# Kernel tuning notes

Measured on AMD Instinct MI355X. Metric: run time of the kernel, lower is better.

Reference implementation:

```python
import jax, jax.numpy as jnp
import numpy as np
from jax import lax

DN = ('NCHW', 'OIHW', 'NCHW')

def binarize(w):
    # torch: w.sign().add(0.5).sign() maps w<0 -> -1, w>=0 -> +1 (0 -> +1)
    return jnp.where(w < 0, -1.0, 1.0).astype(w.dtype)

def bconv(x, w, b, dil):
    wb = binarize(w)
    y = lax.conv_general_dilated(x, wb, window_strides=(1, 1), padding='SAME',
                                 rhs_dilation=dil, dimension_numbers=DN)
    return y + b[None, :, None, None]

def setup_inputs() -> dict:
    key = jax.random.key(0)
    ks = jax.random.split(key, 9)
    C = 256
    Co = C // 4
    x = jax.random.normal(ks[0], (16, C, 128, 128), dtype=jnp.float32)
    w1 = jax.random.normal(ks[1], (Co, C, 1, 5), dtype=jnp.float32) * 0.05
    w2 = jax.random.normal(ks[2], (Co, C, 1, 5), dtype=jnp.float32) * 0.05
    w3 = jax.random.normal(ks[3], (Co, C, 5, 1), dtype=jnp.float32) * 0.05
    w4 = jax.random.normal(ks[4], (Co, C, 5, 1), dtype=jnp.float32) * 0.05
    b1 = jax.random.normal(ks[5], (Co,), dtype=jnp.float32) * 0.01
    b2 = jax.random.normal(ks[6], (Co,), dtype=jnp.float32) * 0.01
    b3 = jax.random.normal(ks[7], (Co,), dtype=jnp.float32) * 0.01
    b4 = jax.random.normal(ks[8], (Co,), dtype=jnp.float32) * 0.01
    return {'x': x, 'w1': w1, 'b1': b1, 'w2': w2, 'b2': b2,
            'w3': w3, 'b3': b3, 'w4': w4, 'b4': b4}

def reference(x, w1, b1, w2, b2, w3, b3, w4, b4):
    out1 = bconv(x, w1, b1, (1, 1))  # (1,5) dil 1
    out2 = bconv(x, w2, b2, (2, 2))  # (1,5) dil 2 (only W dim matters, H kernel=1)
    out3 = bconv(x, w3, b3, (1, 1))  # (5,1) dil 1
    out4 = bconv(x, w4, b4, (2, 2))  # (5,1) dil 2
    return jnp.concatenate([out1, out2, out3, out4], axis=1)
```

## Files before the change

### kernel.cpp

```cpp
#include <hip/hip_runtime.h>

typedef _Float16 half8  __attribute__((ext_vector_type(8)));
typedef float    floatx4 __attribute__((ext_vector_type(4)));

#define HW      128
#define CIN     256
#define NCHUNK  8
#define HALO_W  24
#define HALO_H  16
#define PITCH   20

__global__ void prep_weights(const float* __restrict__ w1,
                             const float* __restrict__ w2,
                             const float* __restrict__ w3,
                             const float* __restrict__ w4,
                             _Float16* __restrict__ wp)
{
    int idx  = blockIdx.x * 256 + threadIdx.x;
    int ci   = idx & 255;
    int rest = idx >> 8;
    int co   = rest & 63;
    int bt   = rest >> 6;
    int t    = bt % 5;
    int b    = bt / 5;
    const float* w = (b == 0) ? w1 : (b == 1) ? w2 : (b == 2) ? w3 : w4;
    float v = w[(co * 256 + ci) * 5 + t];
    wp[idx] = (v < 0.0f) ? (_Float16)(-1.0f) : (_Float16)(1.0f);
}

__global__ __launch_bounds__(256, 2)
void bconv_mfma(const float* __restrict__ x,
                const _Float16* __restrict__ wp,
                const float* __restrict__ bb1,
                const float* __restrict__ bb2,
                const float* __restrict__ bb3,
                const float* __restrict__ bb4,
                float* __restrict__ out)
{
    __shared__ __align__(16) unsigned int xs[HALO_H * HALO_W * PITCH];
    __shared__ float bias_s[256];

    const int tid  = threadIdx.x;
    const int w0t  = blockIdx.x * 16;
    const int h0t  = blockIdx.y * 8;
    const int nimg = blockIdx.z;

    {
        int br = tid >> 6, i = tid & 63;
        const float* bp = (br == 0) ? bb1 : (br == 1) ? bb2 : (br == 2) ? bb3 : bb4;
        bias_s[tid] = bp[i];
    }

    const int lane = tid & 63;
    const int wave = tid >> 6;
    const int quad = lane >> 4;
    const int wl   = lane & 15;

    floatx4 acc[4][8];
    #pragma unroll
    for (int m = 0; m < 4; ++m)
        #pragma unroll
        for (int n = 0; n < 8; ++n)
            acc[m][n] = (floatx4){0.f, 0.f, 0.f, 0.f};

    const int  dil   = (wave & 1) + 1;
    const bool horiz = (wave < 2);

    for (int chunk = 0; chunk < NCHUNK; ++chunk) {
        __syncthreads();

        #pragma unroll
        for (int s = 0; s < 6; ++s) {
            int u   = s * 256 + tid;
            int f   = u % 6;
            int g   = u / 6;
            int hh  = g & 15;
            int cp  = g >> 4;
            int ci0 = chunk * 32 + cp * 2;
            int hg  = h0t - 4 + hh;
            int wg  = w0t - 4 + f * 4;
            floatx4 v0 = {0.f,0.f,0.f,0.f}, v1 = {0.f,0.f,0.f,0.f};
            if (hg >= 0 && hg < HW && wg >= 0 && wg <= HW - 4) {
                const floatx4* p = (const floatx4*)(x + ((nimg * CIN + ci0) * HW + hg) * HW + wg);
                v0 = p[0];
                v1 = p[(HW * HW) / 4];
            }
            int pixb = hh * HALO_W + f * 4;
            #pragma unroll
            for (int i = 0; i < 4; ++i) {
                xs[(pixb + i) * PITCH + cp] =
                    __builtin_bit_cast(unsigned int,
                        __builtin_amdgcn_cvt_pkrtz(v0[i], v1[i]));
            }
        }
        __syncthreads();

        #pragma unroll
        for (int t = 0; t < 5; ++t) {
            half8 B[8];
            #pragma unroll
            for (int n = 0; n < 8; ++n) {
                int hh, ww;
                if (horiz) { hh = n + 4;                  ww = wl + 4 + (t - 2) * dil; }
                else       { hh = n + 4 + (t - 2) * dil;  ww = wl + 4; }
                B[n] = *(const half8*)&xs[(hh * HALO_W + ww) * PITCH + quad * 4];
            }
            #pragma unroll
            for (int m = 0; m < 4; ++m) {
                half8 A = *(const half8*)(wp +
                    (((wave * 5 + t) * 64 + m * 16 + wl) * 256 + chunk * 32 + quad * 8));
                #pragma unroll
                for (int n = 0; n < 8; ++n)
                    acc[m][n] = __builtin_amdgcn_mfma_f32_16x16x32_f16(A, B[n], acc[m][n], 0, 0, 0);
            }
        }
    }

    float bv[4][4];
    #pragma unroll
    for (int m = 0; m < 4; ++m)
        #pragma unroll
        for (int r = 0; r < 4; ++r)
            bv[m][r] = bias_s[wave * 64 + m * 16 + quad * 4 + r];

    #pragma unroll
    for (int m = 0; m < 4; ++m) {
        #pragma unroll
        for (int n = 0; n < 8; ++n) {
            int co   = wave * 64 + m * 16 + quad * 4;
            int base = ((nimg * 256 + co) * HW + (h0t + n)) * HW + w0t + wl;
            #pragma unroll
            for (int r = 0; r < 4; ++r)
                out[base + r * HW * HW] = acc[m][n][r] + bv[m][r];
        }
    }
}

extern "C" void kernel_launch(void* const* d_in, const int* in_sizes, int n_in,
                              void* d_out, int out_size, void* d_ws, size_t ws_size,
                              hipStream_t stream)
{
    (void)in_sizes; (void)n_in; (void)out_size; (void)ws_size;
    const float* x  = (const float*)d_in[0];
    const float* w1 = (const float*)d_in[1];
    const float* b1 = (const float*)d_in[2];
    const float* w2 = (const float*)d_in[3];
    const float* b2 = (const float*)d_in[4];
    const float* w3 = (const float*)d_in[5];
    const float* b3 = (const float*)d_in[6];
    const float* w4 = (const float*)d_in[7];
    const float* b4 = (const float*)d_in[8];
    float*    out = (float*)d_out;
    _Float16* wp  = (_Float16*)d_ws;

    prep_weights<<<1280, 256, 0, stream>>>(w1, w2, w3, w4, wp);

    dim3 grid(128 / 16, 128 / 8, 16);
    bconv_mfma<<<grid, dim3(256), 0, stream>>>(x, wp, b1, b2, b3, b4, out);
}
```

Baseline: 668.3 us.

## Split blocks by conv orientation, prefetch next chunk into registers, swizzle LDS

Each block now handles either the horizontal or the vertical branches, so the halo it loads is only one-sided (24x8 or 16x16 pixels) instead of the full 24x16 square. This removes the redundant loads of the old layout. The next channel chunk's global loads go into registers before the MFMA loop, overlapping memory latency with compute. Adding an XOR swizzle to the LDS layout is meant to reduce bank conflicts. Each wave's accumulators shrink to 4x4, which with launch bounds raised to 3 targets higher occupancy; in exchange the grid doubles and the A-weight loads are repeated across more blocks.

Result: slower. 1.050 ms (+57.1%).

```diff
diff --git a/kernel.cpp b/kernel.cpp
--- a/kernel.cpp
+++ b/kernel.cpp
@@ -3,12 +3,11 @@
 typedef _Float16 half8  __attribute__((ext_vector_type(8)));
 typedef float    floatx4 __attribute__((ext_vector_type(4)));
 
-#define HW      128
-#define CIN     256
-#define NCHUNK  8
-#define HALO_W  24
-#define HALO_H  16
-#define PITCH   20
+#define HW 128
+
+__device__ __forceinline__ int lds_word(int px, int cp) {
+    return px * 20 + (cp ^ (4 * ((px >> 3) & 3)));
+}
 
 __global__ void prep_weights(const float* __restrict__ w1,
                              const float* __restrict__ w2,
@@ -28,7 +27,7 @@
     wp[idx] = (v < 0.0f) ? (_Float16)(-1.0f) : (_Float16)(1.0f);
 }
 
-__global__ __launch_bounds__(256, 2)
+__global__ __launch_bounds__(256, 3)
 void bconv_mfma(const float* __restrict__ x,
                 const _Float16* __restrict__ wp,
                 const float* __restrict__ bb1,
@@ -37,12 +36,13 @@
                 const float* __restrict__ bb4,
                 float* __restrict__ out)
 {
-    __shared__ __align__(16) unsigned int xs[HALO_H * HALO_W * PITCH];
+    __shared__ __align__(16) unsigned int xs[5120];
     __shared__ float bias_s[256];
 
     const int tid  = threadIdx.x;
-    const int w0t  = blockIdx.x * 16;
-    const int h0t  = blockIdx.y * 8;
+    const int type = blockIdx.x & 1;
+    const int w0   = (blockIdx.x >> 1) * 16;
+    const int h0   = blockIdx.y * 8;
     const int nimg = blockIdx.z;
 
     {
@@ -51,66 +51,95 @@
         bias_s[tid] = bp[i];
     }
 
-    const int lane = tid & 63;
-    const int wave = tid >> 6;
-    const int quad = lane >> 4;
-    const int wl   = lane & 15;
+    const int lane   = tid & 63;
+    const int wave   = tid >> 6;
+    const int bi     = wave >> 1;
+    const int half   = wave & 1;
+    const int branch = type * 2 + bi;
+    const int dil    = bi + 1;
+    const int quad   = lane >> 4;
+    const int wl     = lane & 15;
 
-    floatx4 acc[4][8];
+    floatx4 acc[4][4];
     #pragma unroll
     for (int m = 0; m < 4; ++m)
         #pragma unroll
-        for (int n = 0; n < 8; ++n)
+        for (int n = 0; n < 4; ++n)
             acc[m][n] = (floatx4){0.f, 0.f, 0.f, 0.f};
 
-    const int  dil   = (wave & 1) + 1;
-    const bool horiz = (wave < 2);
+    const int NT = type ? 4 : 3;
+    int s_px[4], s_cp[4];
+    const float* s_ptr[4];
+    bool s_ok[4];
+    for (int s = 0; s < 4; ++s) {
+        int u = s * 256 + tid;
+        int f, hh, cp, wg, hg, rowpx;
+        if (type == 0) { f = u % 6;  hh = (u / 6) & 7;   cp = u / 48; wg = w0 - 4 + f * 4; hg = h0 + hh;     rowpx = 24; }
+        else           { f = u & 3;  hh = (u >> 2) & 15; cp = u >> 6; wg = w0 + f * 4;     hg = h0 - 4 + hh; rowpx = 16; }
+        if (cp > 15) cp = 15;
+        s_px[s]  = hh * rowpx + f * 4;
+        s_cp[s]  = cp;
+        s_ok[s]  = (wg >= 0) && (wg <= HW - 4) && (hg >= 0) && (hg < HW);
+        s_ptr[s] = x + (((long)(nimg * 256 + cp * 2) * HW + hg) * HW + wg);
+    }
 
-    for (int chunk = 0; chunk < NCHUNK; ++chunk) {
+    floatx4 R[8];
+
+    {
+        const int coff = 0;
+        for (int s = 0; s < NT; ++s) {
+            floatx4 a = {0.f,0.f,0.f,0.f}, b = {0.f,0.f,0.f,0.f};
+            if (s_ok[s]) {
+                const floatx4* p = (const floatx4*)(s_ptr[s] + coff);
+                a = p[0];
+                b = p[(HW * HW) / 4];
+            }
+            R[2 * s] = a; R[2 * s + 1] = b;
+        }
+    }
+
+    for (int c = 0; c < 8; ++c) {
         __syncthreads();
-
-        #pragma unroll
-        for (int s = 0; s < 6; ++s) {
-            int u   = s * 256 + tid;
-            int f   = u % 6;
-            int g   = u / 6;
-            int hh  = g & 15;
-            int cp  = g >> 4;
-            int ci0 = chunk * 32 + cp * 2;
-            int hg  = h0t - 4 + hh;
-            int wg  = w0t - 4 + f * 4;
-            floatx4 v0 = {0.f,0.f,0.f,0.f}, v1 = {0.f,0.f,0.f,0.f};
-            if (hg >= 0 && hg < HW && wg >= 0 && wg <= HW - 4) {
-                const floatx4* p = (const floatx4*)(x + ((nimg * CIN + ci0) * HW + hg) * HW + wg);
-                v0 = p[0];
-                v1 = p[(HW * HW) / 4];
-            }
-            int pixb = hh * HALO_W + f * 4;
+        for (int s = 0; s < NT; ++s) {
+            int base = s_px[s], cp = s_cp[s];
             #pragma unroll
-            for (int i = 0; i < 4; ++i) {
-                xs[(pixb + i) * PITCH + cp] =
+            for (int i = 0; i < 4; ++i)
+                xs[lds_word(base + i, cp)] =
                     __builtin_bit_cast(unsigned int,
-                        __builtin_amdgcn_cvt_pkrtz(v0[i], v1[i]));
-            }
+                        __builtin_amdgcn_cvt_pkrtz(R[2 * s][i], R[2 * s + 1][i]));
         }
         __syncthreads();
 
+        if (c < 7) {
+            const int coff = (c + 1) * 32 * HW * HW;
+            for (int s = 0; s < NT; ++s) {
+                floatx4 a = {0.f,0.f,0.f,0.f}, b = {0.f,0.f,0.f,0.f};
+                if (s_ok[s]) {
+                    const floatx4* p = (const floatx4*)(s_ptr[s] + coff);
+                    a = p[0];
+                    b = p[(HW * HW) / 4];
+                }
+                R[2 * s] = a; R[2 * s + 1] = b;
+            }
+        }
+
         #pragma unroll
         for (int t = 0; t < 5; ++t) {
-            half8 B[8];
+            half8 B[4];
             #pragma unroll
-            for (int n = 0; n < 8; ++n) {
-                int hh, ww;
-                if (horiz) { hh = n + 4;                  ww = wl + 4 + (t - 2) * dil; }
-                else       { hh = n + 4 + (t - 2) * dil;  ww = wl + 4; }
-                B[n] = *(const half8*)&xs[(hh * HALO_W + ww) * PITCH + quad * 4];
+            for (int n = 0; n < 4; ++n) {
+                int row = half * 4 + n;
+                int px;
+                if (type == 0) px = row * 24 + (wl + 4 + (t - 2) * dil);
+                else           px = (row + 4 + (t - 2) * dil) * 16 + wl;
+                B[n] = *(const half8*)&xs[lds_word(px, quad * 4)];
             }
             #pragma unroll
             for (int m = 0; m < 4; ++m) {
                 half8 A = *(const half8*)(wp +
-                    (((wave * 5 + t) * 64 + m * 16 + wl) * 256 + chunk * 32 + quad * 8));
+                    (((branch * 5 + t) * 64 + m * 16 + wl) * 256 + c * 32 + quad * 8));
                 #pragma unroll
-                for (int n = 0; n < 8; ++n)
+                for (int n = 0; n < 4; ++n)
                     acc[m][n] = __builtin_amdgcn_mfma_f32_16x16x32_f16(A, B[n], acc[m][n], 0, 0, 0);
             }
         }
@@ -121,14 +150,15 @@
     for (int m = 0; m < 4; ++m)
         #pragma unroll
         for (int r = 0; r < 4; ++r)
-            bv[m][r] = bias_s[wave * 64 + m * 16 + quad * 4 + r];
+            bv[m][r] = bias_s[branch * 64 + m * 16 + quad * 4 + r];
 
     #pragma unroll
     for (int m = 0; m < 4; ++m) {
         #pragma unroll
-        for (int n = 0; n < 8; ++n) {
-            int co   = wave * 64 + m * 16 + quad * 4;
-            int base = ((nimg * 256 + co) * HW + (h0t + n)) * HW + w0t + wl;
+        for (int n = 0; n < 4; ++n) {
+            int co = branch * 64 + m * 16 + quad * 4;
+            int h  = h0 + half * 4 + n;
+            int base = ((nimg * 256 + co) * HW + h) * HW + w0 + wl;
             #pragma unroll
             for (int r = 0; r < 4; ++r)
                 out[base + r * HW * HW] = acc[m][n][r] + bv[m][r];
@@ -155,6 +185,6 @@
 
     prep_weights<<<1280, 256, 0, stream>>>(w1, w2, w3, w4, wp);
 
-    dim3 grid(128 / 16, 128 / 8, 16);
+    dim3 grid(16, 16, 16);
     bconv_mfma<<<grid, dim3(256), 0, stream>>>(x, wp, b1, b2, b3, b4, out);
 }
```
